# Optimization experiments

Hardware: AMD Instinct MI355X
Metric: run time of the kernel (lower is better)

## Reference

```python
import jax, jax.numpy as jnp
import numpy as np

N_VERTS = 5000
N_FACES = 10000
BATCH = 2
N_PTS = 8192
OUTER_LOOP = 4
INNER_LOOP = 50
SOLVE_SCALE = 10.0
ADAM_LR = 0.01
B1, B2, EPS = 0.9, 0.999, 1e-8


def _normalize(x, eps=1e-12):
    # torch.nn.functional.normalize(p=2, dim=-1)
    n = jnp.linalg.norm(x, axis=-1, keepdims=True)
    return x / jnp.maximum(n, eps)


def _interp_bary(tri, vw):
    # tri: [M,3,3] per-point triangle attributes, vw: [M,2] barycentric (u,v)
    bary = jnp.concatenate([vw, 1.0 - vw[:, :1] - vw[:, 1:2]], axis=-1)  # [M,3]
    return jnp.einsum('mij,mi->mj', tri, bary)


def _solve_delta_vwd(qV, fid, vw, mesh_V, mesh_F, mesh_N):
    # Newton-like correspondence solve via unrolled Adam (solve_delta_vwd).
    tri_idx = mesh_F[fid]          # [M,3]
    tri_V = mesh_V[tri_idx]        # [M,3,3]
    tri_N = mesh_N[tri_idx]        # [M,3,3]
    d0 = jnp.linalg.norm(_interp_bary(tri_V, vw) - qV, axis=-1)
    delta0 = jnp.concatenate([jnp.zeros_like(vw), d0[:, None]], axis=-1)  # [M,3]
    target = qV * SOLVE_SCALE

    def loss_fn(delta):
        w = vw + delta[:, :2]
        cV = _interp_bary(tri_V, w) * SOLVE_SCALE
        cN = _normalize(_interp_bary(tri_N, w)) * SOLVE_SCALE
        match = cV + cN * delta[:, 2:3]
        return jnp.mean((match - target) ** 2)  # F.mse_loss

    def step(carry, t):
        delta, m, v = carry
        g = jax.grad(loss_fn)(delta)
        m = B1 * m + (1.0 - B1) * g
        v = B2 * v + (1.0 - B2) * g * g
        mhat = m / (1.0 - B1 ** t)
        vhat = v / (1.0 - B2 ** t)
        delta = delta - ADAM_LR * mhat / (jnp.sqrt(vhat) + EPS)
        return (delta, m, v), None

    ts = jnp.arange(1, INNER_LOOP + 1, dtype=qV.dtype)
    zeros = jnp.zeros_like(delta0)
    (delta, _, _), _ = jax.lax.scan(step, (delta0, zeros, zeros), ts)
    return delta


def _forward(verts, mesh_V, mesh_N, mesh_F):
    b, n, _ = verts.shape
    # init_corres_spt: KNN (K=1) of query points against triangle centers
    centers = mesh_V[mesh_F].mean(axis=1)  # [F,3]
    d2 = ((verts ** 2).sum(-1)[..., None]
          + (centers ** 2).sum(-1)[None, None, :]
          - 2.0 * jnp.einsum('bnd,fd->bnf', verts, centers))  # [b,n,F]
    fidx = jnp.argmin(d2, axis=-1)                             # [b,n]
    fid = fidx.reshape(-1)
    qV = verts.reshape(-1, 3)
    vw = jnp.full((b * n, 2), 1.0 / 3.0, dtype=verts.dtype)
    # update_corres_spt (method='uvd'): outer triwalk loop.
    # triwalk is an external CPU mesh-walker; we use the module's documented
    # fallback when triwalk is None: vw <- vw + delta (face index unchanged).
    for _ in range(OUTER_LOOP):
        delta = _solve_delta_vwd(qV, fid, vw, mesh_V, mesh_F, mesh_N)
        vw = vw + delta[:, :2]
    outlier_mask = jnp.zeros((b, n), dtype=bool)  # max_dist = inf
    return fidx, vw.reshape(b, n, 2), outlier_mask


def setup_inputs() -> dict:
    key = jax.random.key(0)
    k1, k2, k3, k4 = jax.random.split(key, 4)
    mesh_V = jax.random.normal(k1, (N_VERTS, 3), dtype=jnp.float32)
    mesh_F = jax.random.randint(k2, (N_FACES, 3), 0, N_VERTS)
    mesh_N = _normalize(jax.random.normal(k3, (N_VERTS, 3), dtype=jnp.float32))
    verts = jax.random.normal(k4, (BATCH, N_PTS, 3), dtype=jnp.float32)
    return {"verts": verts, "mesh_V": mesh_V, "mesh_N": mesh_N, "mesh_F": mesh_F}


def reference(verts, mesh_V, mesh_N, mesh_F):
    return _forward(verts, mesh_V, mesh_N, mesh_F)
```

## Files before the change

kernel.cpp:

```cpp
#include <hip/hip_runtime.h>
#include <math.h>

constexpr int kVerts = 5000;
constexpr int kFaces = 10000;
constexpr int kHalf  = kFaces / 2;
constexpr int kPts   = 16384;
constexpr int kOuter = 4;
constexpr int kInner = 50;

#define SCALE 10.0f

struct BiasTab { float rb1[kInner]; float rb2[kInner]; };
constexpr BiasTab make_tab() {
    BiasTab t{};
    float b1 = 1.0f, b2 = 1.0f;
    for (int i = 0; i < kInner; ++i) {
        b1 *= 0.9f; b2 *= 0.999f;
        t.rb1[i] = 1.0f / (1.0f - b1);
        t.rb2[i] = 1.0f / (1.0f - b2);
    }
    return t;
}
constexpr BiasTab kTab = make_tab();

__global__ __launch_bounds__(256)
void centers_kernel(const float* __restrict__ mesh_V,
                    const int*   __restrict__ mesh_F,
                    float4*      __restrict__ cent)
{
    const int f = blockIdx.x * 256 + threadIdx.x;
    if (f >= kFaces) return;
    const int i0 = mesh_F[f * 3 + 0];
    const int i1 = mesh_F[f * 3 + 1];
    const int i2 = mesh_F[f * 3 + 2];
    const float cx = __fdiv_rn(__fadd_rn(__fadd_rn(mesh_V[i0*3+0], mesh_V[i1*3+0]), mesh_V[i2*3+0]), 3.0f);
    const float cy = __fdiv_rn(__fadd_rn(__fadd_rn(mesh_V[i0*3+1], mesh_V[i1*3+1]), mesh_V[i2*3+1]), 3.0f);
    const float cz = __fdiv_rn(__fadd_rn(__fadd_rn(mesh_V[i0*3+2], mesh_V[i1*3+2]), mesh_V[i2*3+2]), 3.0f);
    const float cc = __fadd_rn(__fadd_rn(__fmul_rn(cx, cx), __fmul_rn(cy, cy)),
                               __fmul_rn(cz, cz));
    cent[f] = make_float4(cx, cy, cz, cc);
}

#define KNN_PARTS 16

__global__ __launch_bounds__(1024)
void knn_kernel(const float* __restrict__ verts,
                const float4* __restrict__ cent,
                float*        __restrict__ ws_d2,
                int*          __restrict__ ws_f)
{
    __shared__ float s_best[1024];
    __shared__ int   s_bestf[1024];

    const int tid  = threadIdx.x;
    const int lane = tid & 63;
    const int part = __builtin_amdgcn_readfirstlane(tid >> 6);
    const int pg   = blockIdx.x >> 1;
    const int half = blockIdx.x & 1;
    const int p    = pg * 64 + lane;

    const float qx = verts[p * 3 + 0];
    const float qy = verts[p * 3 + 1];
    const float qz = verts[p * 3 + 2];
    const float q2 = __fadd_rn(__fadd_rn(__fmul_rn(qx, qx), __fmul_rn(qy, qy)),
                               __fmul_rn(qz, qz));

    const int fbeg = half * kHalf + (part * kHalf) / KNN_PARTS;
    const int fend = half * kHalf + ((part + 1) * kHalf) / KNN_PARTS;

    float bd0 = INFINITY, bd1 = INFINITY, bd2 = INFINITY, bd3 = INFINITY;
    int   bf0 = 0x7fffffff, bf1 = 0x7fffffff, bf2 = 0x7fffffff, bf3 = 0x7fffffff;

#define KNN_EVAL(FF, C, BD, BF)                                                       \
    {                                                                                 \
        const float dot = __fadd_rn(__fadd_rn(__fmul_rn(qx, (C).x),                   \
                                              __fmul_rn(qy, (C).y)),                  \
                                    __fmul_rn(qz, (C).z));                            \
        const float d2 = __fsub_rn(__fadd_rn(q2, (C).w), __fmul_rn(2.0f, dot));       \
        if (d2 < (BD)) { (BD) = d2; (BF) = (FF); }                                    \
    }

    int f = fbeg;
#pragma unroll 4
    for (; f + 4 <= fend; f += 4) {
        const float4 c0 = cent[f + 0];
        const float4 c1 = cent[f + 1];
        const float4 c2 = cent[f + 2];
        const float4 c3 = cent[f + 3];
        KNN_EVAL(f + 0, c0, bd0, bf0);
        KNN_EVAL(f + 1, c1, bd1, bf1);
        KNN_EVAL(f + 2, c2, bd2, bf2);
        KNN_EVAL(f + 3, c3, bd3, bf3);
    }
    for (; f < fend; ++f) {
        const float4 c0 = cent[f];
        KNN_EVAL(f, c0, bd0, bf0);
    }
#undef KNN_EVAL

    if (bd1 < bd0 || (bd1 == bd0 && bf1 < bf0)) { bd0 = bd1; bf0 = bf1; }
    if (bd3 < bd2 || (bd3 == bd2 && bf3 < bf2)) { bd2 = bd3; bf2 = bf3; }
    if (bd2 < bd0 || (bd2 == bd0 && bf2 < bf0)) { bd0 = bd2; bf0 = bf2; }

    s_best[tid]  = bd0;
    s_bestf[tid] = bf0;
    __syncthreads();
    if (part == 0) {
        float best  = bd0;
        int   bestf = bf0;
        for (int k = 1; k < KNN_PARTS; ++k) {
            const float ob = s_best[tid + 64 * k];
            const int   of = s_bestf[tid + 64 * k];
            if (ob < best || (ob == best && of < bestf)) { best = ob; bestf = of; }
        }
        ws_d2[half * kPts + p] = best;
        ws_f [half * kPts + p] = bestf;
    }
}

__global__ __launch_bounds__(64)
void solve_kernel(const float* __restrict__ verts,
                  const float* __restrict__ mesh_V,
                  const float* __restrict__ mesh_N,
                  const int*   __restrict__ mesh_F,
                  const float* __restrict__ ws_d2,
                  const int*   __restrict__ ws_f,
                  float*       __restrict__ out)
{
    const int p = blockIdx.x * 64 + threadIdx.x;

    const float da = ws_d2[p];
    const float db = ws_d2[kPts + p];
    const int   fa = ws_f[p];
    const int   fb = ws_f[kPts + p];
    const int   f  = (db < da) ? fb : fa;
    out[p] = (float)f;

    const float qx = verts[p * 3 + 0];
    const float qy = verts[p * 3 + 1];
    const float qz = verts[p * 3 + 2];

    const int i0 = mesh_F[f * 3 + 0];
    const int i1 = mesh_F[f * 3 + 1];
    const int i2 = mesh_F[f * 3 + 2];

    const float V0x = mesh_V[i0*3+0], V0y = mesh_V[i0*3+1], V0z = mesh_V[i0*3+2];
    const float V1x = mesh_V[i1*3+0], V1y = mesh_V[i1*3+1], V1z = mesh_V[i1*3+2];
    const float V2x = mesh_V[i2*3+0], V2y = mesh_V[i2*3+1], V2z = mesh_V[i2*3+2];
    const float N0x = mesh_N[i0*3+0], N0y = mesh_N[i0*3+1], N0z = mesh_N[i0*3+2];
    const float N1x = mesh_N[i1*3+0], N1y = mesh_N[i1*3+1], N1z = mesh_N[i1*3+2];
    const float N2x = mesh_N[i2*3+0], N2y = mesh_N[i2*3+1], N2z = mesh_N[i2*3+2];

    const float E0x = V0x - V2x, E0y = V0y - V2y, E0z = V0z - V2z;
    const float E1x = V1x - V2x, E1y = V1y - V2y, E1z = V1z - V2z;
    const float F0x = N0x - N2x, F0y = N0y - N2y, F0z = N0z - N2z;
    const float F1x = N1x - N2x, F1y = N1y - N2y, F1z = N1z - N2z;

    const float tx = qx * SCALE, ty = qy * SCALE, tz = qz * SCALE;
    const float GS = 2.0f / (3.0f * 16384.0f);
    const float B1 = 0.9f,  ONE_M_B1 = 1.0f - 0.9f;
    const float B2 = 0.999f, ONE_M_B2 = 1.0f - 0.999f;

    float vwu = 1.0f / 3.0f, vwv = 1.0f / 3.0f;

    for (int outer = 0; outer < kOuter; ++outer) {
        const float bw0 = (1.0f - vwu) - vwv;
        const float px = ((vwu * V0x + vwv * V1x) + bw0 * V2x);
        const float py = ((vwu * V0y + vwv * V1y) + bw0 * V2y);
        const float pz = ((vwu * V0z + vwv * V1z) + bw0 * V2z);
        const float dx = px - qx, dy = py - qy, dz = pz - qz;
        const float d0 = __builtin_amdgcn_sqrtf((dx * dx + dy * dy) + dz * dz);

        float du = 0.0f, dv = 0.0f, dd = d0;
        float mAu = 0.0f, mAv = 0.0f, mAd = 0.0f;
        float vAu = 0.0f, vAv = 0.0f, vAd = 0.0f;

#pragma unroll
        for (int it = 0; it < kInner; ++it) {
            const float bu = vwu + du;
            const float bv = vwv + dv;
            const float bw = (1.0f - bu) - bv;

            const float cVx = ((bu * V0x + bv * V1x) + bw * V2x) * SCALE;
            const float cVy = ((bu * V0y + bv * V1y) + bw * V2y) * SCALE;
            const float cVz = ((bu * V0z + bv * V1z) + bw * V2z) * SCALE;

            const float nrx = (bu * N0x + bv * N1x) + bw * N2x;
            const float nry = (bu * N0y + bv * N1y) + bw * N2y;
            const float nrz = (bu * N0z + bv * N1z) + bw * N2z;
            const float nn  = (nrx * nrx + nry * nry) + nrz * nrz;
            const float inv = __builtin_amdgcn_rsqf(nn);
            const float nhx = nrx * inv, nhy = nry * inv, nhz = nrz * inv;
            const float cNx = nhx * SCALE, cNy = nhy * SCALE, cNz = nhz * SCALE;

            const float rx = (cVx + cNx * dd) - tx;
            const float ry = (cVy + cNy * dd) - ty;
            const float rz = (cVz + cNz * dd) - tz;

            const float rv0  = (rx * E0x + ry * E0y) + rz * E0z;
            const float rv1  = (rx * E1x + ry * E1y) + rz * E1z;
            const float rn0  = (rx * F0x + ry * F0y) + rz * F0z;
            const float rn1  = (rx * F1x + ry * F1y) + rz * F1z;
            const float nf0  = (nhx * F0x + nhy * F0y) + nhz * F0z;
            const float nf1  = (nhx * F1x + nhy * F1y) + nhz * F1z;
            const float nr_r = (nhx * rx + nhy * ry) + nhz * rz;

            const float gu = GS * (SCALE * rv0 + (dd * SCALE) * ((rn0 - nr_r * nf0) * inv));
            const float gv = GS * (SCALE * rv1 + (dd * SCALE) * ((rn1 - nr_r * nf1) * inv));
            const float gd = GS * (SCALE * nr_r);

            mAu = B1 * mAu + ONE_M_B1 * gu;
            mAv = B1 * mAv + ONE_M_B1 * gv;
            mAd = B1 * mAd + ONE_M_B1 * gd;
            vAu = B2 * vAu + ONE_M_B2 * (gu * gu);
            vAv = B2 * vAv + ONE_M_B2 * (gv * gv);
            vAd = B2 * vAd + ONE_M_B2 * (gd * gd);

            const float rb1 = kTab.rb1[it];
            const float rb2 = kTab.rb2[it];
            const float su = __builtin_amdgcn_rsqf(vAu * rb2 + 1e-16f);
            const float sv = __builtin_amdgcn_rsqf(vAv * rb2 + 1e-16f);
            const float sd = __builtin_amdgcn_rsqf(vAd * rb2 + 1e-16f);
            du -= 0.01f * (mAu * rb1) * su;
            dv -= 0.01f * (mAv * rb1) * sv;
            dd -= 0.01f * (mAd * rb1) * sd;
        }
        vwu += du;
        vwv += dv;
    }

    out[kPts + 2 * p + 0] = vwu;
    out[kPts + 2 * p + 1] = vwv;
    out[3 * kPts + p]     = 0.0f;
}

extern "C" void kernel_launch(void* const* d_in, const int* in_sizes, int n_in,
                              void* d_out, int out_size, void* d_ws, size_t ws_size,
                              hipStream_t stream) {
    const float* verts  = (const float*)d_in[0];
    const float* mesh_V = (const float*)d_in[1];
    const float* mesh_N = (const float*)d_in[2];
    const int*   mesh_F = (const int*)d_in[3];
    float* out = (float*)d_out;

    float4* ws_cent = (float4*)d_ws;
    float*  ws_d2   = (float*)((char*)d_ws + kFaces * sizeof(float4));
    int*    ws_f    = (int*)((char*)ws_d2 + 2 * kPts * sizeof(float));

    hipLaunchKernelGGL(centers_kernel, dim3((kFaces + 255) / 256), dim3(256), 0, stream,
                       mesh_V, mesh_F, ws_cent);
    hipLaunchKernelGGL(knn_kernel,     dim3(2 * kPts / 64), dim3(1024), 0, stream,
                       verts, ws_cent, ws_d2, ws_f);
    hipLaunchKernelGGL(solve_kernel,   dim3(kPts / 64), dim3(64), 0, stream,
                       verts, mesh_V, mesh_N, mesh_F, ws_d2, ws_f, out);
}
```

Baseline: 139.8 us.

## Register-block KNN over four query points per lane and split faces into quarters

The KNN kernel now has each lane evaluate four query points against every centroid load, and each block covers 256 points and one quarter of the faces instead of 64 points and one half. The factor 2 is folded into the query coordinates ahead of time, removing a multiply per pair. The goal is to reuse each centroid load across more points, cutting global/L1 traffic per distance evaluation, and to trim ALU work. In exchange, register pressure and the shared-memory reduction grow, the block count drops to 256, and the solve kernel merges four partial results instead of two.

Result: slower. 145.5 us (+4.1%).

```diff
diff --git a/kernel.cpp b/kernel.cpp
--- a/kernel.cpp
+++ b/kernel.cpp
@@ -1,14 +1,21 @@
 #include <hip/hip_runtime.h>
 #include <math.h>
+#include <stdint.h>
 
 constexpr int kVerts = 5000;
 constexpr int kFaces = 10000;
-constexpr int kHalf  = kFaces / 2;
 constexpr int kPts   = 16384;
 constexpr int kOuter = 4;
 constexpr int kInner = 50;
 
 #define SCALE 10.0f
+
+#define KNN_WAVES 16
+#define KNN_FQ    4
+constexpr int kQuarter     = kFaces / KNN_FQ;
+constexpr int kPtsPerLane  = 4;
+constexpr int kPtsPerBlock = 64 * kPtsPerLane;
+constexpr int kPtGroups    = kPts / kPtsPerBlock;
 
 struct BiasTab { float rb1[kInner]; float rb2[kInner]; };
 constexpr BiasTab make_tab() {
@@ -41,80 +48,109 @@
     cent[f] = make_float4(cx, cy, cz, cc);
 }
 
-#define KNN_PARTS 16
-
 __global__ __launch_bounds__(1024)
 void knn_kernel(const float* __restrict__ verts,
                 const float4* __restrict__ cent,
                 float*        __restrict__ ws_d2,
                 int*          __restrict__ ws_f)
 {
-    __shared__ float s_best[1024];
-    __shared__ int   s_bestf[1024];
+    __shared__ float s_best [KNN_WAVES * kPtsPerBlock];
+    __shared__ int   s_bestf[KNN_WAVES * kPtsPerBlock];
 
     const int tid  = threadIdx.x;
     const int lane = tid & 63;
-    const int part = __builtin_amdgcn_readfirstlane(tid >> 6);
-    const int pg   = blockIdx.x >> 1;
-    const int half = blockIdx.x & 1;
-    const int p    = pg * 64 + lane;
-
-    const float qx = verts[p * 3 + 0];
-    const float qy = verts[p * 3 + 1];
-    const float qz = verts[p * 3 + 2];
-    const float q2 = __fadd_rn(__fadd_rn(__fmul_rn(qx, qx), __fmul_rn(qy, qy)),
-                               __fmul_rn(qz, qz));
-
-    const int fbeg = half * kHalf + (part * kHalf) / KNN_PARTS;
-    const int fend = half * kHalf + ((part + 1) * kHalf) / KNN_PARTS;
-
-    float bd0 = INFINITY, bd1 = INFINITY, bd2 = INFINITY, bd3 = INFINITY;
-    int   bf0 = 0x7fffffff, bf1 = 0x7fffffff, bf2 = 0x7fffffff, bf3 = 0x7fffffff;
-
-#define KNN_EVAL(FF, C, BD, BF)                                                       \
+    const int wv   = __builtin_amdgcn_readfirstlane(tid >> 6);
+    const int pg   = blockIdx.x >> 2;
+    const int fq   = blockIdx.x & 3;
+
+    float dqx[kPtsPerLane], dqy[kPtsPerLane], dqz[kPtsPerLane], q2[kPtsPerLane];
+#pragma unroll
+    for (int k = 0; k < kPtsPerLane; ++k) {
+        const int p = pg * kPtsPerBlock + k * 64 + lane;
+        const float qx = verts[p * 3 + 0];
+        const float qy = verts[p * 3 + 1];
+        const float qz = verts[p * 3 + 2];
+        q2[k] = __fadd_rn(__fadd_rn(__fmul_rn(qx, qx), __fmul_rn(qy, qy)),
+                          __fmul_rn(qz, qz));
+        dqx[k] = __fmul_rn(2.0f, qx);
+        dqy[k] = __fmul_rn(2.0f, qy);
+        dqz[k] = __fmul_rn(2.0f, qz);
+    }
+
+    const int qbeg = fq * kQuarter;
+    const int fbeg = qbeg + (wv * kQuarter) / KNN_WAVES;
+    const int fend = qbeg + ((wv + 1) * kQuarter) / KNN_WAVES;
+
+    float bd[kPtsPerLane][2];
+    int   bf[kPtsPerLane][2];
+#pragma unroll
+    for (int k = 0; k < kPtsPerLane; ++k) {
+        bd[k][0] = INFINITY; bd[k][1] = INFINITY;
+        bf[k][0] = 0x7fffffff; bf[k][1] = 0x7fffffff;
+    }
+
+#define KNN_EVAL(FF, C, K, A)                                                         \
     {                                                                                 \
-        const float dot = __fadd_rn(__fadd_rn(__fmul_rn(qx, (C).x),                   \
-                                              __fmul_rn(qy, (C).y)),                  \
-                                    __fmul_rn(qz, (C).z));                            \
-        const float d2 = __fsub_rn(__fadd_rn(q2, (C).w), __fmul_rn(2.0f, dot));       \
-        if (d2 < (BD)) { (BD) = d2; (BF) = (FF); }                                    \
+        const float dot2 = __fadd_rn(__fadd_rn(__fmul_rn(dqx[K], (C).x),              \
+                                               __fmul_rn(dqy[K], (C).y)),             \
+                                     __fmul_rn(dqz[K], (C).z));                       \
+        const float d2 = __fsub_rn(__fadd_rn(q2[K], (C).w), dot2);                    \
+        if (d2 < bd[K][A]) { bd[K][A] = d2; bf[K][A] = (FF); }                        \
     }
 
     int f = fbeg;
-#pragma unroll 4
-    for (; f + 4 <= fend; f += 4) {
+#pragma unroll 1
+    for (; f + 8 <= fend; f += 8) {
         const float4 c0 = cent[f + 0];
         const float4 c1 = cent[f + 1];
         const float4 c2 = cent[f + 2];
         const float4 c3 = cent[f + 3];
-        KNN_EVAL(f + 0, c0, bd0, bf0);
-        KNN_EVAL(f + 1, c1, bd1, bf1);
-        KNN_EVAL(f + 2, c2, bd2, bf2);
-        KNN_EVAL(f + 3, c3, bd3, bf3);
+        const float4 c4 = cent[f + 4];
+        const float4 c5 = cent[f + 5];
+        const float4 c6 = cent[f + 6];
+        const float4 c7 = cent[f + 7];
+#pragma unroll
+        for (int k = 0; k < kPtsPerLane; ++k) {
+            KNN_EVAL(f + 0, c0, k, 0);
+            KNN_EVAL(f + 1, c1, k, 1);
+            KNN_EVAL(f + 2, c2, k, 0);
+            KNN_EVAL(f + 3, c3, k, 1);
+            KNN_EVAL(f + 4, c4, k, 0);
+            KNN_EVAL(f + 5, c5, k, 1);
+            KNN_EVAL(f + 6, c6, k, 0);
+            KNN_EVAL(f + 7, c7, k, 1);
+        }
     }
     for (; f < fend; ++f) {
         const float4 c0 = cent[f];
-        KNN_EVAL(f, c0, bd0, bf0);
+#pragma unroll
+        for (int k = 0; k < kPtsPerLane; ++k)
+            KNN_EVAL(f, c0, k, 0);
     }
 #undef KNN_EVAL
 
-    if (bd1 < bd0 || (bd1 == bd0 && bf1 < bf0)) { bd0 = bd1; bf0 = bf1; }
-    if (bd3 < bd2 || (bd3 == bd2 && bf3 < bf2)) { bd2 = bd3; bf2 = bf3; }
-    if (bd2 < bd0 || (bd2 == bd0 && bf2 < bf0)) { bd0 = bd2; bf0 = bf2; }
-
-    s_best[tid]  = bd0;
-    s_bestf[tid] = bf0;
+#pragma unroll
+    for (int k = 0; k < kPtsPerLane; ++k) {
+        if (bd[k][1] < bd[k][0] || (bd[k][1] == bd[k][0] && bf[k][1] < bf[k][0])) {
+            bd[k][0] = bd[k][1]; bf[k][0] = bf[k][1];
+        }
+        s_best [wv * kPtsPerBlock + k * 64 + lane] = bd[k][0];
+        s_bestf[wv * kPtsPerBlock + k * 64 + lane] = bf[k][0];
+    }
     __syncthreads();
-    if (part == 0) {
-        float best  = bd0;
-        int   bestf = bf0;
-        for (int k = 1; k < KNN_PARTS; ++k) {
-            const float ob = s_best[tid + 64 * k];
-            const int   of = s_bestf[tid + 64 * k];
-            if (ob < best || (ob == best && of < bestf)) { best = ob; bestf = of; }
-        }
-        ws_d2[half * kPts + p] = best;
-        ws_f [half * kPts + p] = bestf;
+
+    if (tid < kPtsPerBlock) {
+        float best  = s_best[tid];
+        int   bestf = s_bestf[tid];
+#pragma unroll
+        for (int w = 1; w < KNN_WAVES; ++w) {
+            const float ob = s_best [w * kPtsPerBlock + tid];
+            const int   of = s_bestf[w * kPtsPerBlock + tid];
+            if (ob < best) { best = ob; bestf = of; }
+        }
+        const int p = pg * kPtsPerBlock + tid;
+        ws_d2[fq * kPts + p] = best;
+        ws_f [fq * kPts + p] = bestf;
     }
 }
 
@@ -129,11 +165,14 @@
 {
     const int p = blockIdx.x * 64 + threadIdx.x;
 
-    const float da = ws_d2[p];
-    const float db = ws_d2[kPts + p];
-    const int   fa = ws_f[p];
-    const int   fb = ws_f[kPts + p];
-    const int   f  = (db < da) ? fb : fa;
+    float bdm = ws_d2[p];
+    int   f   = ws_f[p];
+#pragma unroll
+    for (int q = 1; q < KNN_FQ; ++q) {
+        const float d  = ws_d2[q * kPts + p];
+        const int   ff = ws_f [q * kPts + p];
+        if (d < bdm) { bdm = d; f = ff; }
+    }
     out[p] = (float)f;
 
     const float qx = verts[p * 3 + 0];
@@ -245,11 +284,11 @@
 
     float4* ws_cent = (float4*)d_ws;
     float*  ws_d2   = (float*)((char*)d_ws + kFaces * sizeof(float4));
-    int*    ws_f    = (int*)((char*)ws_d2 + 2 * kPts * sizeof(float));
+    int*    ws_f    = (int*)((char*)ws_d2 + KNN_FQ * kPts * sizeof(float));
 
     hipLaunchKernelGGL(centers_kernel, dim3((kFaces + 255) / 256), dim3(256), 0, stream,
                        mesh_V, mesh_F, ws_cent);
-    hipLaunchKernelGGL(knn_kernel,     dim3(2 * kPts / 64), dim3(1024), 0, stream,
+    hipLaunchKernelGGL(knn_kernel,     dim3(kPtGroups * KNN_FQ), dim3(1024), 0, stream,
                        verts, ws_cent, ws_d2, ws_f);
     hipLaunchKernelGGL(solve_kernel,   dim3(kPts / 64), dim3(64), 0, stream,
                        verts, mesh_V, mesh_N, mesh_F, ws_d2, ws_f, out);
```
